# Optimization experiments

Hardware: AMD Instinct MI355X
Metric: run time of the kernel (lower is better)

The kernel has to match this reference:

```python
import jax, jax.numpy as jnp
import numpy as np

INPUT_SIZE = 512
LATENT = 256
NUM_PROTOTYPES = 128
NUM_CLASSES = 8
PC = NUM_PROTOTYPES // NUM_CLASSES  # prototypes per class
EPS = 1e-4
LOG_MIN = float(np.log(1e-8))  # clamp bounds for logVar


def setup_inputs() -> dict:
    key = jax.random.key(0)
    ks = jax.random.split(key, 12)
    B = 16384
    s = 0.05
    return {
        "x_tab": jax.random.normal(ks[0], (B, INPUT_SIZE), jnp.float32),
        "t": jax.random.randint(ks[1], (B,), 0, NUM_CLASSES),
        "prototype_vectors": jax.random.normal(ks[2], (NUM_PROTOTYPES, LATENT), jnp.float32),
        "W1": jax.random.normal(ks[3], (2 * LATENT, INPUT_SIZE), jnp.float32) * s,
        "b1": jnp.zeros((2 * LATENT,), jnp.float32),
        "W2": jax.random.normal(ks[4], (2 * LATENT, 2 * LATENT), jnp.float32) * s,
        "b2": jnp.zeros((2 * LATENT,), jnp.float32),
        "Wd1": jax.random.normal(ks[5], (LATENT, LATENT), jnp.float32) * s,
        "bd1": jnp.zeros((LATENT,), jnp.float32),
        "Wd2": jax.random.normal(ks[6], (INPUT_SIZE, LATENT), jnp.float32) * s,
        "bd2": jnp.zeros((INPUT_SIZE,), jnp.float32),
        "W_last": jax.random.normal(ks[7], (1, NUM_PROTOTYPES), jnp.float32) * s,
    }


def reference(x_tab, t, prototype_vectors, W1, b1, W2, b2, Wd1, bd1, Wd2, bd2, W_last):
    B = x_tab.shape[0]
    # encoder MLP: Linear -> ReLU -> Linear, output [B, 2*latent]
    h = jnp.maximum(x_tab @ W1.T + b1, 0.0)
    conv = h @ W2.T + b2
    mu = conv[:, :LATENT]
    logVar = jnp.clip(conv[:, LATENT:], LOG_MIN, -LOG_MIN)
    z = mu  # test=True path: z = mu (deterministic)

    # per-sample indices of the prototypes of the correct class: [B, PC]
    idx = t[:, None] * PC + jnp.arange(PC)[None, :]
    protos = prototype_vectors[idx]  # [B, PC, L] gather

    # cdist (p=2) + log-similarity
    diff = z[:, None, :] - protos  # [B, PC, L]
    d = jnp.sqrt(jnp.sum(diff * diff, axis=-1))  # [B, PC]
    sim = jnp.log((d + 1.0) / (d + EPS))

    # scatter into full [B, P] sparse sim tensor
    full_sim = jnp.zeros((B, NUM_PROTOTYPES), x_tab.dtype).at[
        jnp.arange(B)[:, None], idx].set(sim)

    # KL(N(mu, exp(logVar/2)) || N(p, 1)) per-dim, mean over latent
    var = jnp.exp(logVar)
    kl = jnp.mean(-0.5 * logVar[:, None, :]
                  + 0.5 * (var[:, None, :] + diff * diff)
                  - 0.5, axis=-1)  # [B, PC]
    klw = kl * sim
    mask = (klw > 0).astype(sim.dtype)
    kl_loss = jnp.mean(jnp.sum(klw, axis=1) / jnp.sum(sim * mask, axis=1))

    out = full_sim @ W_last.T  # [B, 1]

    # decoder: Linear -> ReLU -> Linear -> tanh
    dh = jnp.maximum(z @ Wd1.T + bd1, 0.0)
    decoded = jnp.tanh(dh @ Wd2.T + bd2)

    # ortho loss over per-class prototype blocks
    pk = prototype_vectors.reshape(NUM_CLASSES, PC, LATENT)
    pk = pk - jnp.mean(pk, axis=1, keepdims=True)
    gram = jnp.einsum('cil,cjl->cij', pk, pk) - jnp.eye(PC, dtype=pk.dtype)
    ortho_loss = jnp.mean(jnp.sqrt(jnp.sum(gram * gram, axis=(1, 2))))

    return out, decoded, kl_loss, ortho_loss
```

## Files before the change

kernel.cpp:

```cpp
#include <hip/hip_runtime.h>
#include <math.h>

typedef unsigned short u16;
typedef unsigned int   u32;
typedef _Float16 f16;
typedef f16   f16x4 __attribute__((ext_vector_type(4)));
typedef f16   f16x8 __attribute__((ext_vector_type(8)));
typedef float f32x4 __attribute__((ext_vector_type(4)));

#define B_ROWS 16384
#define PC 16
#define EPS_SIM 1e-4f
#define LOG_MIN_F (-18.420680743952367f)
#define KL_IDX  (B_ROWS + B_ROWS * 512)
#define OR_IDX  (KL_IDX + 1)

#define GLD16(gp, lp) __builtin_amdgcn_global_load_lds( \
    (const __attribute__((address_space(1))) void*)(gp), \
    (__attribute__((address_space(3))) void*)(lp), 16, 0, 0)

__device__ __forceinline__ void conv4(const float* __restrict__ src,
                                      f16* __restrict__ dst, int i)
{
    float4 v = ((const float4*)src)[i];
    f16x4 o = { (f16)v.x, (f16)v.y, (f16)v.z, (f16)v.w };
    ((f16x4*)dst)[i] = o;
}

__global__ __launch_bounds__(256)
void prep_kernel(const float* __restrict__ x,   const float* __restrict__ W1,
                 const float* __restrict__ W2,  const float* __restrict__ Wd1,
                 const float* __restrict__ Wd2, const float* __restrict__ protos,
                 f16* __restrict__ x_h,  f16* __restrict__ W1h,
                 f16* __restrict__ W2h,  f16* __restrict__ Wd1h,
                 f16* __restrict__ Wd2h, f16* __restrict__ ph,
                 float* __restrict__ pnorm, float* __restrict__ opart,
                 float* __restrict__ S, float* __restrict__ Mn,
                 float* __restrict__ out)
{
    __shared__ float pk[PC][257];
    __shared__ float red[256];
    int blk = blockIdx.x, t = threadIdx.x;

    if (blk < 8) {
        int c = blk;
        for (int i = t; i < PC * 256; i += 256)
            pk[i >> 8][i & 255] = protos[c * PC * 256 + i];
        __syncthreads();
        float mean = 0.f;
#pragma unroll
        for (int i = 0; i < PC; ++i) mean += pk[i][t];
        mean *= (1.f / (float)PC);
#pragma unroll
        for (int i = 0; i < PC; ++i) pk[i][t] -= mean;
        __syncthreads();
        int i = t >> 4, j = t & 15;
        float gg = 0.f;
#pragma unroll 8
        for (int l = 0; l < 256; ++l) gg = fmaf(pk[i][l], pk[j][l], gg);
        gg -= (i == j) ? 1.f : 0.f;
        red[t] = gg * gg;
        __syncthreads();
        for (int s = 128; s; s >>= 1) { if (t < s) red[t] += red[t + s]; __syncthreads(); }
        if (t == 0) opart[c] = sqrtf(red[0]);
        return;
    }
    int b2 = blk - 8;
    if (b2 < 8192)         conv4(x,   x_h,  b2 * 256 + t);
    else if (b2 < 8448)    conv4(W1,  W1h,  (b2 - 8192) * 256 + t);
    else if (b2 < 8704)    conv4(W2,  W2h,  (b2 - 8448) * 256 + t);
    else if (b2 < 8768)    conv4(Wd1, Wd1h, (b2 - 8704) * 256 + t);
    else if (b2 < 8896)    conv4(Wd2, Wd2h, (b2 - 8768) * 256 + t);
    else if (b2 < 8928)    conv4(protos, ph, (b2 - 8896) * 256 + t);
    else if (b2 < 8930) {
        int tt = (b2 - 8928) * 256 + t;
        int row = tt >> 2, q = tt & 3;
        const float* pr = protos + (size_t)row * 256 + q * 64;
        float s = 0.f;
#pragma unroll
        for (int j = 0; j < 16; ++j) {
            float4 v = *(const float4*)(pr + j * 4);
            float r0 = (float)(f16)v.x, r1 = (float)(f16)v.y;
            float r2 = (float)(f16)v.z, r3 = (float)(f16)v.w;
            s = fmaf(r0, r0, s); s = fmaf(r1, r1, s);
            s = fmaf(r2, r2, s); s = fmaf(r3, r3, s);
        }
        s += __shfl_xor(s, 1, 64);
        s += __shfl_xor(s, 2, 64);
        if (q == 0) pnorm[row] = s;
    } else {
        int i = (b2 - 8930) * 256 + t;
        S[i] = 0.f; Mn[i] = 0.f;
        if (i == 0) out[KL_IDX] = 0.f;
    }
}

template<int MODE, int KK>
__global__ __launch_bounds__(256, 2)
void gemm_mfma(const f16* __restrict__ A, const f16* __restrict__ B,
               const f16* __restrict__ P, const float* __restrict__ bias,
               f16* __restrict__ C16, float* __restrict__ Cf,
               float* __restrict__ Srow, float* __restrict__ Mnorm,
               const int* __restrict__ tcls, const float* __restrict__ pnorm,
               const float* __restrict__ Wlast, const float* __restrict__ opart,
               float* __restrict__ out, float* __restrict__ kl_out,
               int ldc)
{
    __shared__ __align__(16) f16 LA[128][32];
    __shared__ __align__(16) f16 LB[128][32];
    __shared__ float klacc;

    const int t = threadIdx.x, lane = t & 63, wave = t >> 6;
    const int wm = wave >> 1, wn = wave & 1;
    const int bm = blockIdx.x * 128;
    const int y  = blockIdx.y;
    const bool proto = (MODE == 5) && (y == 2);
    const int bn  = y * 128;
    const int bnB = proto ? 0 : bn;
    const f16* Bp = proto ? P : B;
    const int rA = lane & 15, g = lane >> 4;
    const int srow = lane >> 2, cp = lane & 3;

    if (t == 0) klacc = 0.f;

    f32x4 acc[4][4];
    const f32x4 z4 = {0.f, 0.f, 0.f, 0.f};
#pragma unroll
    for (int i = 0; i < 4; ++i)
#pragma unroll
        for (int j = 0; j < 4; ++j) acc[i][j] = z4;

    auto stage = [&](int kt) {
#pragma unroll
        for (int s = 0; s < 2; ++s) {
            int row = wave * 32 + s * 16 + srow;
            int lc  = (cp - (row >> 1)) & 3;
            GLD16(A  + (size_t)(bm  + row) * KK + kt * 32 + lc * 8,
                  &LA[wave * 32 + s * 16][0]);
            GLD16(Bp + (size_t)(bnB + row) * KK + kt * 32 + lc * 8,
                  &LB[wave * 32 + s * 16][0]);
        }
    };

    constexpr int T = KK / 32;
    stage(0);
    for (int tk = 0; tk < T; ++tk) {
        __syncthreads();

        f16x8 a[4], b[4];
#pragma unroll
        for (int i = 0; i < 4; ++i) {
            int m = wm * 64 + i * 16 + rA;
            int c = ((g + (m >> 1)) & 3) * 8;
            a[i] = *(const f16x8*)&LA[m][c];
            int n = wn * 64 + i * 16 + rA;
            int cn = ((g + (n >> 1)) & 3) * 8;
            b[i] = *(const f16x8*)&LB[n][cn];
        }

        __syncthreads();
        if (tk + 1 < T) stage(tk + 1);

#pragma unroll
        for (int i = 0; i < 4; ++i)
#pragma unroll
            for (int j = 0; j < 4; ++j)
                acc[i][j] = __builtin_amdgcn_mfma_f32_16x16x32_f16(a[i], b[j], acc[i][j], 0, 0, 0);
    }

    if (proto) {
        float pn[4], wl[4];
#pragma unroll
        for (int j = 0; j < 4; ++j) {
            int col = wn * 64 + j * 16 + rA;
            pn[j] = pnorm[col];
            wl[j] = Wlast[col];
        }
#pragma unroll
        for (int i = 0; i < 4; ++i)
#pragma unroll
            for (int r = 0; r < 4; ++r) {
                int row = bm + wm * 64 + i * 16 + g * 4 + r;
                int cls = tcls[row];
                int jsel = cls & 3;
                bool owner = ((cls >> 2) == wn);
                float cv = 0.f, pnv = 0.f, wlv = 0.f;
#pragma unroll
                for (int j = 0; j < 4; ++j) {
                    bool sel = (j == jsel);
                    cv  = sel ? acc[i][j][r] : cv;
                    pnv = sel ? pn[j] : pnv;
                    wlv = sel ? wl[j] : wlv;
                }
                float dd  = fmaxf(Mnorm[row] + pnv - 2.f * cv, 0.f);
                float d   = sqrtf(dd);
                float sim = __logf((d + 1.0f) / (d + EPS_SIM));
                float kl  = Srow[row] + dd * (0.5f / 256.f);
                float klw = kl * sim;
                float num = klw;
                float den = (klw > 0.0f) ? sim : 0.0f;
                float ov  = sim * wlv;
                num += __shfl_xor(num, 1, 64); den += __shfl_xor(den, 1, 64); ov += __shfl_xor(ov, 1, 64);
                num += __shfl_xor(num, 2, 64); den += __shfl_xor(den, 2, 64); ov += __shfl_xor(ov, 2, 64);
                num += __shfl_xor(num, 4, 64); den += __shfl_xor(den, 4, 64); ov += __shfl_xor(ov, 4, 64);
                num += __shfl_xor(num, 8, 64); den += __shfl_xor(den, 8, 64); ov += __shfl_xor(ov, 8, 64);
                if (owner && rA == 0) {
                    out[row] = ov;
                    atomicAdd(&klacc, num / den);
                }
            }
        __syncthreads();
        if (t == 0) {
            atomicAdd(kl_out, klacc * (1.f / (float)B_ROWS));
            if (blockIdx.x == 0) {
                float o = 0.f;
#pragma unroll
                for (int c = 0; c < 8; ++c) o += opart[c];
                out[OR_IDX] = o * (1.f / 8.f);
            }
        }
        return;
    }

    float bv[4];
#pragma unroll
    for (int j = 0; j < 4; ++j) bv[j] = bias[bn + wn * 64 + j * 16 + rA];

    if (MODE == 4 && y >= 2) {
#pragma unroll
        for (int i = 0; i < 4; ++i)
#pragma unroll
            for (int r = 0; r < 4; ++r) {
                int row = bm + wm * 64 + i * 16 + g * 4 + r;
                float s = 0.f;
#pragma unroll
                for (int j = 0; j < 4; ++j) {
                    float lv = acc[i][j][r] + bv[j];
                    lv = fminf(fmaxf(lv, LOG_MIN_F), -LOG_MIN_F);
                    s += 0.5f * __expf(lv) - 0.5f * lv - 0.5f;
                }
                s += __shfl_xor(s, 1, 64); s += __shfl_xor(s, 2, 64);
                s += __shfl_xor(s, 4, 64); s += __shfl_xor(s, 8, 64);
                if (rA == 0) atomicAdd(&Srow[row], s * (1.f / 256.f));
            }
        return;
    }

#pragma unroll
    for (int i = 0; i < 4; ++i)
#pragma unroll
        for (int r = 0; r < 4; ++r) {
            size_t row = bm + wm * 64 + i * 16 + g * 4 + r;
            float sq = 0.f;
#pragma unroll
            for (int j = 0; j < 4; ++j) {
                int col = bn + wn * 64 + j * 16 + rA;
                float v = acc[i][j][r] + bv[j];
                if (MODE == 0 || MODE == 5) v = fmaxf(v, 0.f);
                if (MODE == 3) {
                    float e = __expf(2.f * v);
                    Cf[row * ldc + col] = 1.f - 2.f / (e + 1.f);
                } else {
                    f16 hv = (f16)v;
                    C16[row * ldc + col] = hv;
                    if (MODE == 4) {
                        float vr = (float)hv;
                        sq = fmaf(vr, vr, sq);
                    }
                }
            }
            if (MODE == 4) {
                sq += __shfl_xor(sq, 1, 64); sq += __shfl_xor(sq, 2, 64);
                sq += __shfl_xor(sq, 4, 64); sq += __shfl_xor(sq, 8, 64);
                if (rA == 0) atomicAdd(&Mnorm[row], sq);
            }
        }
}

extern "C" void kernel_launch(void* const* d_in, const int* in_sizes, int n_in,
                              void* d_out, int out_size, void* d_ws, size_t ws_size,
                              hipStream_t stream)
{
    const float* x      = (const float*)d_in[0];
    const int*   tcls   = (const int*)  d_in[1];
    const float* protos = (const float*)d_in[2];
    const float* W1     = (const float*)d_in[3];
    const float* b1     = (const float*)d_in[4];
    const float* W2     = (const float*)d_in[5];
    const float* b2     = (const float*)d_in[6];
    const float* Wd1    = (const float*)d_in[7];
    const float* bd1    = (const float*)d_in[8];
    const float* Wd2    = (const float*)d_in[9];
    const float* bd2    = (const float*)d_in[10];
    const float* Wlast  = (const float*)d_in[11];

    float* out     = (float*)d_out;
    float* decoded = out + B_ROWS;

    f16* h_h = (f16*)decoded;

    f16* wsf  = (f16*)d_ws;
    f16* x_h  = wsf;
    f16* mu_h = wsf + 8388608;
    f16* dh_h = wsf + 12582912;

    float* S = (float*)((char*)d_ws + 33554432);
    f16* w = (f16*)(S + 32768);
    f16 *W1h = w, *W2h = w + 262144, *Wd1h = w + 524288, *Wd2h = w + 589824;
    f16 *ph  = w + 720896;
    float* munorm = (float*)(w + 753664);
    float* pnorm  = munorm + 16384;
    float* opart  = pnorm + 128;

    hipLaunchKernelGGL(prep_kernel, dim3(9002), dim3(256), 0, stream,
                       x, W1, W2, Wd1, Wd2, protos,
                       x_h, W1h, W2h, Wd1h, Wd2h, ph,
                       pnorm, opart, S, munorm, out);

    hipLaunchKernelGGL((gemm_mfma<0, 512>), dim3(128, 4), dim3(256), 0, stream,
                       x_h, W1h, (f16*)nullptr, b1,
                       h_h, (float*)nullptr, (float*)nullptr, (float*)nullptr,
                       (int*)nullptr, (float*)nullptr, (float*)nullptr, (float*)nullptr,
                       (float*)nullptr, (float*)nullptr, 512);
    hipLaunchKernelGGL((gemm_mfma<4, 512>), dim3(128, 4), dim3(256), 0, stream,
                       h_h, W2h, (f16*)nullptr, b2,
                       mu_h, (float*)nullptr, S, munorm,
                       (int*)nullptr, (float*)nullptr, (float*)nullptr, (float*)nullptr,
                       (float*)nullptr, (float*)nullptr, 256);
    hipLaunchKernelGGL((gemm_mfma<5, 256>), dim3(128, 3), dim3(256), 0, stream,
                       mu_h, Wd1h, ph, bd1,
                       dh_h, (float*)nullptr, S, munorm,
                       tcls, pnorm, Wlast, opart,
                       out, out + KL_IDX, 256);
    hipLaunchKernelGGL((gemm_mfma<3, 256>), dim3(128, 4), dim3(256), 0, stream,
                       dh_h, Wd2h, (f16*)nullptr, bd2,
                       (f16*)nullptr, decoded, (float*)nullptr, (float*)nullptr,
                       (int*)nullptr, (float*)nullptr, (float*)nullptr, (float*)nullptr,
                       (float*)nullptr, (float*)nullptr, 512);
}
```

Baseline: 81.31 us.

## Split prototype similarity epilogue out of GEMM into separate finish kernel

```diff
diff --git a/kernel.cpp b/kernel.cpp
--- a/kernel.cpp
+++ b/kernel.cpp
@@ -101,14 +101,10 @@
                const f16* __restrict__ P, const float* __restrict__ bias,
                f16* __restrict__ C16, float* __restrict__ Cf,
                float* __restrict__ Srow, float* __restrict__ Mnorm,
-               const int* __restrict__ tcls, const float* __restrict__ pnorm,
-               const float* __restrict__ Wlast, const float* __restrict__ opart,
-               float* __restrict__ out, float* __restrict__ kl_out,
-               int ldc)
+               f16* __restrict__ Xc, int ldc)
 {
     __shared__ __align__(16) f16 LA[128][32];
     __shared__ __align__(16) f16 LB[128][32];
-    __shared__ float klacc;
 
     const int t = threadIdx.x, lane = t & 63, wave = t >> 6;
     const int wm = wave >> 1, wn = wave & 1;
@@ -121,8 +117,6 @@
     const int rA = lane & 15, g = lane >> 4;
     const int srow = lane >> 2, cp = lane & 3;
 
-    if (t == 0) klacc = 0.f;
-
     f32x4 acc[4][4];
     const f32x4 z4 = {0.f, 0.f, 0.f, 0.f};
 #pragma unroll
@@ -169,56 +163,17 @@
     }
 
     if (proto) {
-        float pn[4], wl[4];
-#pragma unroll
-        for (int j = 0; j < 4; ++j) {
-            int col = wn * 64 + j * 16 + rA;
-            pn[j] = pnorm[col];
-            wl[j] = Wlast[col];
-        }
 #pragma unroll
         for (int i = 0; i < 4; ++i)
 #pragma unroll
             for (int r = 0; r < 4; ++r) {
-                int row = bm + wm * 64 + i * 16 + g * 4 + r;
-                int cls = tcls[row];
-                int jsel = cls & 3;
-                bool owner = ((cls >> 2) == wn);
-                float cv = 0.f, pnv = 0.f, wlv = 0.f;
+                size_t row = bm + wm * 64 + i * 16 + g * 4 + r;
 #pragma unroll
                 for (int j = 0; j < 4; ++j) {
-                    bool sel = (j == jsel);
-                    cv  = sel ? acc[i][j][r] : cv;
-                    pnv = sel ? pn[j] : pnv;
-                    wlv = sel ? wl[j] : wlv;
-                }
-                float dd  = fmaxf(Mnorm[row] + pnv - 2.f * cv, 0.f);
-                float d   = sqrtf(dd);
-                float sim = __logf((d + 1.0f) / (d + EPS_SIM));
-                float kl  = Srow[row] + dd * (0.5f / 256.f);
-                float klw = kl * sim;
-                float num = klw;
-                float den = (klw > 0.0f) ? sim : 0.0f;
-                float ov  = sim * wlv;
-                num += __shfl_xor(num, 1, 64); den += __shfl_xor(den, 1, 64); ov += __shfl_xor(ov, 1, 64);
-                num += __shfl_xor(num, 2, 64); den += __shfl_xor(den, 2, 64); ov += __shfl_xor(ov, 2, 64);
-                num += __shfl_xor(num, 4, 64); den += __shfl_xor(den, 4, 64); ov += __shfl_xor(ov, 4, 64);
-                num += __shfl_xor(num, 8, 64); den += __shfl_xor(den, 8, 64); ov += __shfl_xor(ov, 8, 64);
-                if (owner && rA == 0) {
-                    out[row] = ov;
-                    atomicAdd(&klacc, num / den);
+                    int col = wn * 64 + j * 16 + rA;
+                    Xc[row * 128 + col] = (f16)acc[i][j][r];
                 }
             }
-        __syncthreads();
-        if (t == 0) {
-            atomicAdd(kl_out, klacc * (1.f / (float)B_ROWS));
-            if (blockIdx.x == 0) {
-                float o = 0.f;
-#pragma unroll
-                for (int c = 0; c < 8; ++c) o += opart[c];
-                out[OR_IDX] = o * (1.f / 8.f);
-            }
-        }
         return;
     }
 
@@ -277,6 +232,57 @@
         }
 }
 
+__global__ __launch_bounds__(256)
+void proto_finish(const f16* __restrict__ Xc, const float* __restrict__ Mnorm,
+                  const float* __restrict__ Sr, const int* __restrict__ tcls,
+                  const float* __restrict__ pnorm, const float* __restrict__ Wlast,
+                  const float* __restrict__ opart,
+                  float* __restrict__ out, float* __restrict__ kl_out)
+{
+    __shared__ float pnS[128], wlS[128], red[4];
+    int t = threadIdx.x;
+    if (t < 128) { pnS[t] = pnorm[t]; wlS[t] = Wlast[t]; }
+    __syncthreads();
+
+    int b = blockIdx.x * 256 + t;
+    int cls = tcls[b];
+    float Mn = Mnorm[b], Sb = Sr[b];
+    const f16* xr = Xc + (size_t)b * 128 + cls * 16;
+    f16x8 c0 = *(const f16x8*)xr;
+    f16x8 c1 = *(const f16x8*)(xr + 8);
+
+    float num = 0.f, den = 0.f, ov = 0.f;
+#pragma unroll
+    for (int p = 0; p < 16; ++p) {
+        float c  = (p < 8) ? (float)c0[p] : (float)c1[p - 8];
+        int  ip  = cls * 16 + p;
+        float dd = fmaxf(Mn + pnS[ip] - 2.f * c, 0.f);
+        float d  = sqrtf(dd);
+        float sim = __logf((d + 1.f) / (d + EPS_SIM));
+        float kl  = Sb + dd * (0.5f / 256.f);
+        float klw = kl * sim;
+        num += klw;
+        den += (klw > 0.f) ? sim : 0.f;
+        ov  += sim * wlS[ip];
+    }
+    out[b] = ov;
+
+    float v = num / den;
+#pragma unroll
+    for (int off = 32; off; off >>= 1) v += __shfl_xor(v, off, 64);
+    int lane = t & 63, w = t >> 6;
+    if (lane == 0) red[w] = v;
+    __syncthreads();
+    if (t == 0)
+        atomicAdd(kl_out, (red[0] + red[1] + red[2] + red[3]) * (1.f / (float)B_ROWS));
+    if (blockIdx.x == 0 && t == 0) {
+        float o = 0.f;
+#pragma unroll
+        for (int c8 = 0; c8 < 8; ++c8) o += opart[c8];
+        out[OR_IDX] = o * (1.f / 8.f);
+    }
+}
+
 extern "C" void kernel_launch(void* const* d_in, const int* in_sizes, int n_in,
                               void* d_out, int out_size, void* d_ws, size_t ws_size,
                               hipStream_t stream)
@@ -311,6 +317,7 @@
     float* munorm = (float*)(w + 753664);
     float* pnorm  = munorm + 16384;
     float* opart  = pnorm + 128;
+    f16* Xc = (f16*)((char*)d_ws + 37748736);
 
     hipLaunchKernelGGL(prep_kernel, dim3(9002), dim3(256), 0, stream,
                        x, W1, W2, Wd1, Wd2, protos,
@@ -320,21 +327,20 @@
     hipLaunchKernelGGL((gemm_mfma<0, 512>), dim3(128, 4), dim3(256), 0, stream,
                        x_h, W1h, (f16*)nullptr, b1,
                        h_h, (float*)nullptr, (float*)nullptr, (float*)nullptr,
-                       (int*)nullptr, (float*)nullptr, (float*)nullptr, (float*)nullptr,
-                       (float*)nullptr, (float*)nullptr, 512);
+                       (f16*)nullptr, 512);
     hipLaunchKernelGGL((gemm_mfma<4, 512>), dim3(128, 4), dim3(256), 0, stream,
                        h_h, W2h, (f16*)nullptr, b2,
                        mu_h, (float*)nullptr, S, munorm,
-                       (int*)nullptr, (float*)nullptr, (float*)nullptr, (float*)nullptr,
-                       (float*)nullptr, (float*)nullptr, 256);
+                       (f16*)nullptr, 256);
     hipLaunchKernelGGL((gemm_mfma<5, 256>), dim3(128, 3), dim3(256), 0, stream,
                        mu_h, Wd1h, ph, bd1,
-                       dh_h, (float*)nullptr, S, munorm,
-                       tcls, pnorm, Wlast, opart,
-                       out, out + KL_IDX, 256);
+                       dh_h, (float*)nullptr, (float*)nullptr, (float*)nullptr,
+                       Xc, 256);
+    hipLaunchKernelGGL(proto_finish, dim3(64), dim3(256), 0, stream,
+                       Xc, munorm, S, tcls, pnorm, Wlast, opart,
+                       out, out + KL_IDX);
     hipLaunchKernelGGL((gemm_mfma<3, 256>), dim3(128, 4), dim3(256), 0, stream,
                        dh_h, Wd2h, (f16*)nullptr, bd2,
                        (f16*)nullptr, decoded, (float*)nullptr, (float*)nullptr,
-                       (int*)nullptr, (float*)nullptr, (float*)nullptr, (float*)nullptr,
-                       (float*)nullptr, (float*)nullptr, 512);
-}
+                       (f16*)nullptr, 512);
+}
```

Result: faster. 77.05 us (-5.2%).
